# Kernel optimization log

Measured on AMD Instinct MI355X. Metric: run time of the kernel, lower is better.

## Reference

```python
import jax, jax.numpy as jnp
import numpy as np

B, C, H, W = 32, 512, 32, 32
N = H * W            # seq_len = 1024
HEADS = 8
DH = C // HEADS      # 64
K = 256              # linformer low-rank
EPS = 1e-5


def setup_inputs() -> dict:
    key = jax.random.key(0)
    ks = jax.random.split(key, 10)
    s = 0.02
    return {
        "x": jax.random.normal(ks[0], (B, C, H, W), dtype=jnp.float32),
        "pos": jax.random.normal(ks[1], (1, N, C), dtype=jnp.float32),
        "ln_g": jnp.ones((C,), dtype=jnp.float32),
        "ln_b": jnp.zeros((C,), dtype=jnp.float32),
        "Wq": jax.random.normal(ks[2], (C, C), dtype=jnp.float32) * s,
        "Wk": jax.random.normal(ks[3], (C, C), dtype=jnp.float32) * s,
        "Wv": jax.random.normal(ks[4], (C, C), dtype=jnp.float32) * s,
        "proj_k": jax.random.normal(ks[5], (N, K), dtype=jnp.float32) * s,
        "proj_v": jax.random.normal(ks[6], (N, K), dtype=jnp.float32) * s,
        "Wo": jax.random.normal(ks[7], (C, C), dtype=jnp.float32) * s,
        "bo": jnp.zeros((C,), dtype=jnp.float32),
    }


def reference(x, pos, ln_g, ln_b, Wq, Wk, Wv, proj_k, proj_v, Wo, bo):
    b, c, h, w = x.shape
    n = h * w
    # b c h w -> b (h w) c
    xf = x.reshape(b, c, n).transpose(0, 2, 1) + pos
    # LayerNorm (biased variance, eps=1e-5) + ReLU; dropout = identity (eval)
    mu = xf.mean(-1, keepdims=True)
    var = jnp.var(xf, axis=-1, keepdims=True)
    y = (xf - mu) * jax.lax.rsqrt(var + EPS) * ln_g + ln_b
    y = jax.nn.relu(y)
    # Linformer self-attention
    q = y @ Wq                                   # [b,n,c]
    k_ = jnp.einsum('bnd,nk->bkd', y @ Wk, proj_k)  # [b,K,c]
    v_ = jnp.einsum('bnd,nk->bkd', y @ Wv, proj_v)  # [b,K,c]
    q = q.reshape(b, n, HEADS, DH)
    k_ = k_.reshape(b, K, HEADS, DH)
    v_ = v_.reshape(b, K, HEADS, DH)
    dots = jnp.einsum('bnhd,bkhd->bhnk', q, k_) * (DH ** -0.5)
    attn = jax.nn.softmax(dots, axis=-1)
    out = jnp.einsum('bhnk,bkhd->bnhd', attn, v_).reshape(b, n, c)
    out = out @ Wo + bo
    # residual with (x + pos), then back to b c h w
    out = out + xf
    return out.transpose(0, 2, 1).reshape(b, c, h, w)
```

## Files before the change

kernel.cpp:

```cpp
#include <hip/hip_runtime.h>
#include <hip/hip_bf16.h>
#include <cstdint>

#define BB  32
#define CC  512
#define NN  1024
#define HH  8
#define DHH 64
#define KR  256

using f32x4  = __attribute__((ext_vector_type(4))) float;
using f32x16 = __attribute__((ext_vector_type(16))) float;
using bf16x8 = __attribute__((ext_vector_type(8))) __bf16;
using u32x4  = __attribute__((ext_vector_type(4))) unsigned int;

__device__ __forceinline__ unsigned short f2bf(float f) {
  unsigned int u = __float_as_uint(f);
  u += 0x7fffu + ((u >> 16) & 1u);
  return (unsigned short)(u >> 16);
}

__device__ __forceinline__ unsigned int pknat(float a, float b) {
  unsigned short ua = __builtin_bit_cast(unsigned short, (__bf16)a);
  unsigned short ub = __builtin_bit_cast(unsigned short, (__bf16)b);
  return (unsigned int)ua | ((unsigned int)ub << 16);
}

__device__ __forceinline__ void gload16(const void* gsrc, void* ldst) {
  __builtin_amdgcn_global_load_lds(
      (const __attribute__((address_space(1))) unsigned int*)gsrc,
      (__attribute__((address_space(3))) unsigned int*)ldst, 16, 0, 0);
}

__global__ __launch_bounds__(256) void transcvt_all(
    const float* __restrict__ w0, const float* __restrict__ w1,
    const float* __restrict__ w2, const float* __restrict__ w3,
    const float* __restrict__ p0, const float* __restrict__ p1,
    unsigned short* __restrict__ d0, unsigned short* __restrict__ d1,
    unsigned short* __restrict__ d2, unsigned short* __restrict__ d3,
    unsigned short* __restrict__ e0, unsigned short* __restrict__ e1) {
  const int m = blockIdx.y;
  const float* src = m==0?w0:m==1?w1:m==2?w2:m==3?w3:m==4?p0:p1;
  unsigned short* dst = m==0?d0:m==1?d1:m==2?d2:m==3?d3:m==4?e0:e1;
  const int R = (m < 4) ? 512 : 1024;
  const int logC = (m < 4) ? 9 : 8;
  int idx = blockIdx.x * 256 + threadIdx.x;
  int r = idx >> logC, c = idx & ((1 << logC) - 1);
  dst[(size_t)c * R + r] = f2bf(src[idx]);
}

__global__ __launch_bounds__(256) void ln_relu_kernel(
    const float* __restrict__ x, const float* __restrict__ pos,
    const float* __restrict__ g, const float* __restrict__ bta,
    unsigned short* __restrict__ y, unsigned short* __restrict__ yT) {
  __shared__ float tile[16][516];
  __shared__ float smu[16], srs[16];
  const int b = blockIdx.y, n0 = blockIdx.x * 16;
  const int tid = threadIdx.x;
  const float* xb = x + (size_t)b * CC * NN;

  #pragma unroll
  for (int i = 0; i < 32; ++i) {
    int e = i * 256 + tid;
    int c = e >> 4, nl = e & 15;
    tile[nl][c] = xb[(size_t)c * NN + n0 + nl];
  }
  __syncthreads();

  const int r = tid >> 4, l16 = tid & 15;
  float s = 0.f, s2 = 0.f;
  #pragma unroll
  for (int i = 0; i < 32; ++i) {
    int c = l16 + i * 16;
    float v = tile[r][c] + pos[(size_t)(n0 + r) * CC + c];
    s += v; s2 += v * v;
  }
  #pragma unroll
  for (int d = 1; d < 16; d <<= 1) { s += __shfl_xor(s, d); s2 += __shfl_xor(s2, d); }
  if (l16 == 0) {
    float mu = s * (1.f / 512.f);
    float var = s2 * (1.f / 512.f) - mu * mu;
    smu[r] = mu;
    srs[r] = rsqrtf(var + 1e-5f);
  }
  __syncthreads();

  unsigned short* yb = y + ((size_t)b * NN + n0) * CC;
  #pragma unroll
  for (int rr = 0; rr < 16; ++rr) {
    float mu = smu[rr], rs = srs[rr];
    #pragma unroll
    for (int c = tid; c < CC; c += 256) {
      float v = tile[rr][c] + pos[(size_t)(n0 + rr) * CC + c];
      float o = (v - mu) * rs * g[c] + bta[c];
      o = o > 0.f ? o : 0.f;
      yb[(size_t)rr * CC + c] = f2bf(o);
      tile[rr][c] = o;
    }
  }
  __syncthreads();

  unsigned short* ytb = yT + (size_t)b * CC * NN + n0;
  #pragma unroll
  for (int cc = tid; cc < CC; cc += 256) {
    unsigned int pk8[8];
    #pragma unroll
    for (int p = 0; p < 8; ++p)
      pk8[p] = (unsigned int)f2bf(tile[2 * p][cc]) |
               ((unsigned int)f2bf(tile[2 * p + 1][cc]) << 16);
    *reinterpret_cast<uint4*>(&ytb[(size_t)cc * NN])     = *reinterpret_cast<uint4*>(&pk8[0]);
    *reinterpret_cast<uint4*>(&ytb[(size_t)cc * NN + 8]) = *reinterpret_cast<uint4*>(&pk8[4]);
  }
}

template <int MODE>
__global__ __launch_bounds__(256) void gemm_tn(
    const unsigned short* __restrict__ A, int lda, long long strideA,
    const unsigned short* __restrict__ Bt, int ldb, long long strideB,
    unsigned short* __restrict__ Cb, long long strideC,
    int Nn, int Kk, int TB,
    const float* __restrict__ xres, const float* __restrict__ posres,
    const float* __restrict__ bias, float* __restrict__ outF) {
  __shared__ __align__(16) unsigned short aL[2][128 * 64];
  __shared__ __align__(16) unsigned short bL[2][128 * 64];
  const int mb = blockIdx.x * 128, nb = blockIdx.y * 128, zb = blockIdx.z;
  A  += (size_t)strideA * zb;
  Bt += (size_t)strideB * zb;
  if (MODE == 0 || MODE == 1) Cb += (size_t)strideC * zb;
  const int tid  = threadIdx.x;
  const int lane = tid & 63;
  const int wave = tid >> 6;
  const int wm = (wave >> 1) * 64, wn = (wave & 1) * 64;
  const int sr = lane >> 3;
  const int scw = lane & 7;
  f32x4 acc[4][4] = {};

  auto stage = [&](int buf, int k0) {
    #pragma unroll
    for (int i = 0; i < 4; ++i) {
      int row = wave * 32 + i * 8 + sr;
      int ca = scw ^ (row & 7);
      gload16(&A [(size_t)(mb + row) * lda + k0 + ca * 8], &aL[buf][(wave * 32 + i * 8) * 64]);
      gload16(&Bt[(size_t)(nb + row) * ldb + k0 + ca * 8], &bL[buf][(wave * 32 + i * 8) * 64]);
    }
  };

  const int nt = Kk >> 6;
  stage(0, 0);
  __syncthreads();

  for (int t = 0; t < nt; ++t) {
    const int buf = t & 1;
    if (t + 1 < nt) stage(buf ^ 1, (t + 1) << 6);

    bf16x8 af[2][4], bfv[2][4];
    #pragma unroll
    for (int ks = 0; ks < 2; ++ks)
      #pragma unroll
      for (int i = 0; i < 4; ++i) {
        int ra = wm + i * 16 + (lane & 15);
        int rb = wn + i * 16 + (lane & 15);
        int kc = ks * 4 + (lane >> 4);
        af[ks][i]  = *reinterpret_cast<const bf16x8*>(&aL[buf][ra * 64 + (kc ^ (ra & 7)) * 8]);
        bfv[ks][i] = *reinterpret_cast<const bf16x8*>(&bL[buf][rb * 64 + (kc ^ (rb & 7)) * 8]);
      }
    #pragma unroll
    for (int ks = 0; ks < 2; ++ks)
      #pragma unroll
      for (int i = 0; i < 4; ++i)
        #pragma unroll
        for (int j = 0; j < 4; ++j)
          acc[i][j] = __builtin_amdgcn_mfma_f32_16x16x32_bf16(af[ks][i], bfv[ks][j], acc[i][j], 0, 0, 0);
    __syncthreads();
  }

  #pragma unroll
  for (int i = 0; i < 4; ++i) {
    const int r0 = mb + wm + i * 16 + ((lane >> 4) << 2);
    #pragma unroll
    for (int j = 0; j < 4; ++j) {
      const int col = nb + wn + j * 16 + (lane & 15);
      if (MODE == 0) {
        #pragma unroll
        for (int t = 0; t < 4; ++t)
          Cb[(size_t)(r0 + t) * Nn + col] = f2bf(acc[i][j][t]);
      } else if (MODE == 1) {
        unsigned int lo = (unsigned int)f2bf(acc[i][j][0]) | ((unsigned int)f2bf(acc[i][j][1]) << 16);
        unsigned int hi = (unsigned int)f2bf(acc[i][j][2]) | ((unsigned int)f2bf(acc[i][j][3]) << 16);
        size_t addr = (size_t)col * TB + (r0 % TB);
        uint2 u; u.x = lo; u.y = hi;
        *reinterpret_cast<uint2*>(&Cb[addr]) = u;
      } else {
        const int bb = r0 >> 10, t0 = r0 & 1023;
        const size_t base = ((size_t)bb * CC + col) * NN + t0;
        float4 xv = *reinterpret_cast<const float4*>(&xres[base]);
        float bcol = bias[col];
        float4 ov;
        ov.x = acc[i][j][0] + bcol + xv.x + posres[(size_t)(t0 + 0) * CC + col];
        ov.y = acc[i][j][1] + bcol + xv.y + posres[(size_t)(t0 + 1) * CC + col];
        ov.z = acc[i][j][2] + bcol + xv.z + posres[(size_t)(t0 + 2) * CC + col];
        ov.w = acc[i][j][3] + bcol + xv.w + posres[(size_t)(t0 + 3) * CC + col];
        *reinterpret_cast<float4*>(&outF[base]) = ov;
      }
    }
  }
}

__global__ __launch_bounds__(256, 2) void attn_kernel(
    const unsigned short* __restrict__ q,
    const unsigned short* __restrict__ kB,
    const unsigned short* __restrict__ vT,
    unsigned short* __restrict__ O) {
  __shared__ __align__(16) unsigned short smem[32768];
  const int wgid = blockIdx.x;
  const int grp  = wgid & 255;
  const int tg   = wgid >> 8;
  const int h = grp & 7, b = grp >> 3;
  const int wave = threadIdx.x >> 6, lane = threadIdx.x & 63;
  const int t32 = lane & 31, g2 = lane >> 5;
  const int tokb = tg * 128 + wave * 32;

  const unsigned short* qp = q + ((size_t)(b * NN + tokb + t32)) * CC + h * DHH + g2 * 8;
  bf16x8 qf[4];
  #pragma unroll
  for (int st = 0; st < 4; ++st)
    qf[st] = *reinterpret_cast<const bf16x8*>(qp + (size_t)st * 16);

  {
    const unsigned short* kb = kB + ((size_t)b * KR) * CC + h * DHH;
    const int r0w = wave * 64;
    #pragma unroll
    for (int i = 0; i < 8; ++i) {
      int row = r0w + i * 8 + (lane >> 3);
      int sc  = (lane & 7) ^ (row & 7);
      gload16(kb + (size_t)row * CC + sc * 8, &smem[(r0w + i * 8) * 64]);
    }
    const unsigned short* vb = vT + ((size_t)b * CC + h * DHH) * KR;
    const int v0w = wave * 16;
    #pragma unroll
    for (int i = 0; i < 8; ++i) {
      int row = v0w + i * 2 + (lane >> 5);
      int sc  = (lane & 31) ^ (row & 7);
      gload16(vb + (size_t)row * KR + sc * 8, &smem[16384 + (v0w + i * 2) * 256]);
    }
  }
  __syncthreads();

  f32x16 s8[8] = {};
  #pragma unroll
  for (int t8 = 0; t8 < 8; ++t8) {
    const int row = t8 * 32 + t32;
    #pragma unroll
    for (int st = 0; st < 4; ++st) {
      int ch = (2 * st + g2) ^ (row & 7);
      bf16x8 kf = *reinterpret_cast<const bf16x8*>(&smem[row * 64 + ch * 8]);
      s8[t8] = __builtin_amdgcn_mfma_f32_32x32x16_bf16(kf, qf[st], s8[t8], 0, 0, 0);
    }
  }

  float m = -1e30f;
  #pragma unroll
  for (int t8 = 0; t8 < 8; ++t8)
    #pragma unroll
    for (int r = 0; r < 16; ++r) m = fmaxf(m, s8[t8][r]);
  m = fmaxf(m, __shfl_xor(m, 32));
  const float cexp = 0.125f * 1.44269504088896f;
  float ls = 0.f;
  #pragma unroll
  for (int t8 = 0; t8 < 8; ++t8)
    #pragma unroll
    for (int r = 0; r < 16; ++r) {
      float p = __builtin_amdgcn_exp2f((s8[t8][r] - m) * cexp);
      s8[t8][r] = p;
      ls += p;
    }
  ls += __shfl_xor(ls, 32);
  float rinv = __builtin_amdgcn_rcpf(ls);

  f32x16 o0 = {}, o1 = {};
  #pragma unroll
  for (int t8 = 0; t8 < 8; ++t8) {
    unsigned int pkd[8];
    #pragma unroll
    for (int qq = 0; qq < 4; ++qq) {
      pkd[qq * 2 + 0] = pknat(s8[t8][4 * qq + 0], s8[t8][4 * qq + 1]);
      pkd[qq * 2 + 1] = pknat(s8[t8][4 * qq + 2], s8[t8][4 * qq + 3]);
    }
    #pragma unroll
    for (int a = 0; a < 2; ++a) {
      const int ks = t8 * 2 + a;
      unsigned int xe0 = pkd[4 * a + 0], xe1 = pkd[4 * a + 1];
      unsigned int xo0 = pkd[4 * a + 2], xo1 = pkd[4 * a + 3];
      unsigned int d0 = g2 ? __shfl_xor(xo0, 32) : xe0;
      unsigned int d1 = g2 ? __shfl_xor(xo1, 32) : xe1;
      unsigned int d2 = g2 ? xo0 : __shfl_xor(xe0, 32);
      unsigned int d3 = g2 ? xo1 : __shfl_xor(xe1, 32);
      u32x4 pv_ = {d0, d1, d2, d3};
      bf16x8 pa = __builtin_bit_cast(bf16x8, pv_);
      #pragma unroll
      for (int dt = 0; dt < 2; ++dt) {
        int row = dt * 32 + t32;
        int ch = (2 * ks + g2) ^ (row & 7);
        bf16x8 bv = *reinterpret_cast<const bf16x8*>(&smem[16384 + row * 256 + ch * 8]);
        if (dt == 0) o0 = __builtin_amdgcn_mfma_f32_32x32x16_bf16(pa, bv, o0, 0, 0, 0);
        else         o1 = __builtin_amdgcn_mfma_f32_32x32x16_bf16(pa, bv, o1, 0, 0, 0);
      }
    }
  }

  unsigned short* Ob = O + ((size_t)(b * NN + tokb)) * CC + h * DHH;
  #pragma unroll
  for (int r = 0; r < 16; ++r) {
    int tl = (r & 3) + 8 * (r >> 2) + 4 * g2;
    float rs = __shfl(rinv, tl);
    Ob[(size_t)tl * CC + t32]      = f2bf(o0[r] * rs);
    Ob[(size_t)tl * CC + 32 + t32] = f2bf(o1[r] * rs);
  }
}

extern "C" void kernel_launch(void* const* d_in, const int* in_sizes, int n_in,
                              void* d_out, int out_size, void* d_ws, size_t ws_size,
                              hipStream_t stream) {
  const float* x    = (const float*)d_in[0];
  const float* pos  = (const float*)d_in[1];
  const float* ln_g = (const float*)d_in[2];
  const float* ln_b = (const float*)d_in[3];
  const float* Wq   = (const float*)d_in[4];
  const float* Wk   = (const float*)d_in[5];
  const float* Wv   = (const float*)d_in[6];
  const float* pk   = (const float*)d_in[7];
  const float* pv   = (const float*)d_in[8];
  const float* Wo   = (const float*)d_in[9];
  const float* bo   = (const float*)d_in[10];
  float* out = (float*)d_out;

  unsigned short* ws = (unsigned short*)d_ws;
  size_t off = 0;
  auto alloc = [&](size_t elems) { unsigned short* p = ws + off; off += elems; return p; };
  unsigned short* WqT     = alloc(512 * 512);
  unsigned short* WkT     = alloc(512 * 512);
  unsigned short* WvT     = alloc(512 * 512);
  unsigned short* WoT     = alloc(512 * 512);
  unsigned short* projcat = alloc((size_t)512 * 1024);
  unsigned short* yB      = alloc((size_t)32768 * 512);
  unsigned short* yT      = alloc((size_t)32 * 512 * 1024);
  unsigned short* qB      = alloc((size_t)32768 * 512);
  unsigned short* zB      = alloc((size_t)32 * 512 * 512);
  unsigned short* kBuf    = alloc((size_t)32 * 256 * 512);
  unsigned short* vTB     = alloc((size_t)32 * 512 * 256);
  unsigned short* OB      = alloc((size_t)32768 * 512);

  transcvt_all<<<dim3(1024, 6), 256, 0, stream>>>(
      Wq, Wk, Wv, Wo, pk, pv,
      WqT, WkT, WvT, WoT, projcat, projcat + (size_t)256 * 1024);

  ln_relu_kernel<<<dim3(64, 32), 256, 0, stream>>>(x, pos, ln_g, ln_b, yB, yT);

  gemm_tn<0><<<dim3(256, 4), 256, 0, stream>>>(
      yB, 512, 0, WqT, 512, 0, qB, 0, 512, 512, 0, nullptr, nullptr, nullptr, nullptr);

  gemm_tn<0><<<dim3(4, 4, 32), 256, 0, stream>>>(
      projcat, 1024, 0, yT, 1024, (long long)512 * 1024, zB, (long long)512 * 512,
      512, 1024, 0, nullptr, nullptr, nullptr, nullptr);

  gemm_tn<0><<<dim3(2, 4, 32), 256, 0, stream>>>(
      zB, 512, (long long)512 * 512, WkT, 512, 0, kBuf, (long long)256 * 512,
      512, 512, 0, nullptr, nullptr, nullptr, nullptr);

  gemm_tn<1><<<dim3(2, 4, 32), 256, 0, stream>>>(
      zB + (size_t)256 * 512, 512, (long long)512 * 512, WvT, 512, 0,
      vTB, (long long)512 * 256, 512, 512, 256, nullptr, nullptr, nullptr, nullptr);

  attn_kernel<<<dim3(2048, 1, 1), 256, 0, stream>>>(qB, kBuf, vTB, OB);

  gemm_tn<2><<<dim3(256, 4), 256, 0, stream>>>(
      OB, 512, 0, WoT, 512, 0, nullptr, 0, 512, 512, 0, x, pos, bo, out);
}
```

Measured before the change: 228.6 us.

## Shrink GEMM K-tile, stage epilogues through LDS, transpose output GEMM for coalescing

The GEMM K-step drops from 64 to 32 with a new 4-way swizzle, which cuts LDS use and may allow more resident blocks. MODE 0 and MODE 1 epilogues now stage the bf16 tile in shared memory and write 16-byte coalesced rows instead of scattered 2-byte or 8-byte stores. The output projection swaps its operands so that consecutive lanes map to consecutive tokens, and reads a pre-transposed fp32 pos copy made by a new kernel, so the NCHW residual stores become coalesced. LayerNorm now adds pos into the tile once instead of reading it twice. Grid dimensions are swapped to match the new block-index mapping, and the changes add an extra kernel launch and more loop iterations per GEMM.

```diff
diff --git a/kernel.cpp b/kernel.cpp
--- a/kernel.cpp
+++ b/kernel.cpp
@@ -49,6 +49,13 @@
   dst[(size_t)c * R + r] = f2bf(src[idx]);
 }
 
+__global__ __launch_bounds__(256) void posT_kernel(
+    const float* __restrict__ pos, float* __restrict__ posT) {
+  int idx = blockIdx.x * 256 + threadIdx.x;
+  int c = idx >> 10, n = idx & 1023;
+  posT[idx] = pos[(size_t)n * CC + c];
+}
+
 __global__ __launch_bounds__(256) void ln_relu_kernel(
     const float* __restrict__ x, const float* __restrict__ pos,
     const float* __restrict__ g, const float* __restrict__ bta,
@@ -66,13 +73,18 @@
     tile[nl][c] = xb[(size_t)c * NN + n0 + nl];
   }
   __syncthreads();
+  #pragma unroll
+  for (int i = 0; i < 32; ++i) {
+    int nl = i >> 1, c = (i & 1) * 256 + tid;
+    tile[nl][c] += pos[(size_t)(n0 + nl) * CC + c];
+  }
+  __syncthreads();
 
   const int r = tid >> 4, l16 = tid & 15;
   float s = 0.f, s2 = 0.f;
   #pragma unroll
   for (int i = 0; i < 32; ++i) {
-    int c = l16 + i * 16;
-    float v = tile[r][c] + pos[(size_t)(n0 + r) * CC + c];
+    float v = tile[r][l16 + i * 16];
     s += v; s2 += v * v;
   }
   #pragma unroll
@@ -91,7 +103,7 @@
     float mu = smu[rr], rs = srs[rr];
     #pragma unroll
     for (int c = tid; c < CC; c += 256) {
-      float v = tile[rr][c] + pos[(size_t)(n0 + rr) * CC + c];
+      float v = tile[rr][c];
       float o = (v - mu) * rs * g[c] + bta[c];
       o = o > 0.f ? o : 0.f;
       yb[(size_t)rr * CC + c] = f2bf(o);
@@ -119,11 +131,12 @@
     const unsigned short* __restrict__ Bt, int ldb, long long strideB,
     unsigned short* __restrict__ Cb, long long strideC,
     int Nn, int Kk, int TB,
-    const float* __restrict__ xres, const float* __restrict__ posres,
+    const float* __restrict__ xres, const float* __restrict__ posT,
     const float* __restrict__ bias, float* __restrict__ outF) {
-  __shared__ __align__(16) unsigned short aL[2][128 * 64];
-  __shared__ __align__(16) unsigned short bL[2][128 * 64];
-  const int mb = blockIdx.x * 128, nb = blockIdx.y * 128, zb = blockIdx.z;
+  __shared__ __align__(16) unsigned short sh[17408];
+  unsigned short* aL = sh;
+  unsigned short* bL = sh + 8192;
+  const int nb = blockIdx.x * 128, mb = blockIdx.y * 128, zb = blockIdx.z;
   A  += (size_t)strideA * zb;
   Bt += (size_t)strideB * zb;
   if (MODE == 0 || MODE == 1) Cb += (size_t)strideC * zb;
@@ -131,77 +144,87 @@
   const int lane = tid & 63;
   const int wave = tid >> 6;
   const int wm = (wave >> 1) * 64, wn = (wave & 1) * 64;
-  const int sr = lane >> 3;
-  const int scw = lane & 7;
+  const int sr  = lane >> 2;
+  const int scw = lane & 3;
   f32x4 acc[4][4] = {};
 
   auto stage = [&](int buf, int k0) {
     #pragma unroll
-    for (int i = 0; i < 4; ++i) {
-      int row = wave * 32 + i * 8 + sr;
-      int ca = scw ^ (row & 7);
-      gload16(&A [(size_t)(mb + row) * lda + k0 + ca * 8], &aL[buf][(wave * 32 + i * 8) * 64]);
-      gload16(&Bt[(size_t)(nb + row) * ldb + k0 + ca * 8], &bL[buf][(wave * 32 + i * 8) * 64]);
+    for (int i = 0; i < 2; ++i) {
+      int rbase = wave * 32 + i * 16;
+      int row = rbase + sr;
+      int ca = scw ^ ((row ^ (row >> 2)) & 3);
+      gload16(&A [(size_t)(mb + row) * lda + k0 + ca * 8], &aL[buf * 4096 + rbase * 32]);
+      gload16(&Bt[(size_t)(nb + row) * ldb + k0 + ca * 8], &bL[buf * 4096 + rbase * 32]);
     }
   };
 
-  const int nt = Kk >> 6;
+  const int nt = Kk >> 5;
   stage(0, 0);
   __syncthreads();
 
   for (int t = 0; t < nt; ++t) {
     const int buf = t & 1;
-    if (t + 1 < nt) stage(buf ^ 1, (t + 1) << 6);
-
-    bf16x8 af[2][4], bfv[2][4];
-    #pragma unroll
-    for (int ks = 0; ks < 2; ++ks)
+    if (t + 1 < nt) stage(buf ^ 1, (t + 1) << 5);
+
+    bf16x8 af[4], bfv[4];
+    const int kc = lane >> 4;
+    #pragma unroll
+    for (int i = 0; i < 4; ++i) {
+      int ra = wm + i * 16 + (lane & 15);
+      int rb = wn + i * 16 + (lane & 15);
+      af[i]  = *reinterpret_cast<const bf16x8*>(&aL[buf * 4096 + ra * 32 + (kc ^ ((ra ^ (ra >> 2)) & 3)) * 8]);
+      bfv[i] = *reinterpret_cast<const bf16x8*>(&bL[buf * 4096 + rb * 32 + (kc ^ ((rb ^ (rb >> 2)) & 3)) * 8]);
+    }
+    #pragma unroll
+    for (int i = 0; i < 4; ++i)
       #pragma unroll
-      for (int i = 0; i < 4; ++i) {
-        int ra = wm + i * 16 + (lane & 15);
-        int rb = wn + i * 16 + (lane & 15);
-        int kc = ks * 4 + (lane >> 4);
-        af[ks][i]  = *reinterpret_cast<const bf16x8*>(&aL[buf][ra * 64 + (kc ^ (ra & 7)) * 8]);
-        bfv[ks][i] = *reinterpret_cast<const bf16x8*>(&bL[buf][rb * 64 + (kc ^ (rb & 7)) * 8]);
+      for (int j = 0; j < 4; ++j)
+        acc[i][j] = __builtin_amdgcn_mfma_f32_16x16x32_bf16(af[i], bfv[j], acc[i][j], 0, 0, 0);
+    __syncthreads();
+  }
+
+  if (MODE == 2) {
+    #pragma unroll
+    for (int i = 0; i < 4; ++i) {
+      const int c0 = mb + wm + i * 16 + ((lane >> 4) << 2);
+      #pragma unroll
+      for (int j = 0; j < 4; ++j) {
+        const int col = nb + wn + j * 16 + (lane & 15);
+        const int bcell = col >> 10, t0 = col & 1023;
+        #pragma unroll
+        for (int t = 0; t < 4; ++t) {
+          const int c = c0 + t;
+          const size_t base = ((size_t)bcell * CC + c) * NN + t0;
+          outF[base] = acc[i][j][t] + bias[c] + xres[base] + posT[(size_t)c * NN + t0];
+        }
       }
-    #pragma unroll
-    for (int ks = 0; ks < 2; ++ks)
+    }
+  } else {
+    auto Ct = (unsigned short (*)[136])sh;
+    #pragma unroll
+    for (int i = 0; i < 4; ++i) {
+      const int r0 = wm + i * 16 + ((lane >> 4) << 2);
       #pragma unroll
-      for (int i = 0; i < 4; ++i)
+      for (int j = 0; j < 4; ++j) {
+        const int cl = wn + j * 16 + (lane & 15);
         #pragma unroll
-        for (int j = 0; j < 4; ++j)
-          acc[i][j] = __builtin_amdgcn_mfma_f32_16x16x32_bf16(af[ks][i], bfv[ks][j], acc[i][j], 0, 0, 0);
+        for (int t = 0; t < 4; ++t) {
+          if (MODE == 0) Ct[r0 + t][cl] = f2bf(acc[i][j][t]);
+          else           Ct[cl][r0 + t] = f2bf(acc[i][j][t]);
+        }
+      }
+    }
     __syncthreads();
-  }
-
-  #pragma unroll
-  for (int i = 0; i < 4; ++i) {
-    const int r0 = mb + wm + i * 16 + ((lane >> 4) << 2);
-    #pragma unroll
-    for (int j = 0; j < 4; ++j) {
-      const int col = nb + wn + j * 16 + (lane & 15);
-      if (MODE == 0) {
-        #pragma unroll
-        for (int t = 0; t < 4; ++t)
-          Cb[(size_t)(r0 + t) * Nn + col] = f2bf(acc[i][j][t]);
-      } else if (MODE == 1) {
-        unsigned int lo = (unsigned int)f2bf(acc[i][j][0]) | ((unsigned int)f2bf(acc[i][j][1]) << 16);
-        unsigned int hi = (unsigned int)f2bf(acc[i][j][2]) | ((unsigned int)f2bf(acc[i][j][3]) << 16);
-        size_t addr = (size_t)col * TB + (r0 % TB);
-        uint2 u; u.x = lo; u.y = hi;
-        *reinterpret_cast<uint2*>(&Cb[addr]) = u;
-      } else {
-        const int bb = r0 >> 10, t0 = r0 & 1023;
-        const size_t base = ((size_t)bb * CC + col) * NN + t0;
-        float4 xv = *reinterpret_cast<const float4*>(&xres[base]);
-        float bcol = bias[col];
-        float4 ov;
-        ov.x = acc[i][j][0] + bcol + xv.x + posres[(size_t)(t0 + 0) * CC + col];
-        ov.y = acc[i][j][1] + bcol + xv.y + posres[(size_t)(t0 + 1) * CC + col];
-        ov.z = acc[i][j][2] + bcol + xv.z + posres[(size_t)(t0 + 2) * CC + col];
-        ov.w = acc[i][j][3] + bcol + xv.w + posres[(size_t)(t0 + 3) * CC + col];
-        *reinterpret_cast<float4*>(&outF[base]) = ov;
-      }
+    const int rr = tid >> 4, ch = tid & 15;
+    #pragma unroll
+    for (int it = 0; it < 8; ++it) {
+      const int r = it * 16 + rr;
+      uint4 v = *reinterpret_cast<const uint4*>(&Ct[r][ch * 8]);
+      if (MODE == 0)
+        *reinterpret_cast<uint4*>(&Cb[(size_t)(mb + r) * Nn + nb + ch * 8]) = v;
+      else
+        *reinterpret_cast<uint4*>(&Cb[(size_t)(nb + r) * TB + mb + ch * 8]) = v;
     }
   }
 }
@@ -342,6 +365,7 @@
   unsigned short* WvT     = alloc(512 * 512);
   unsigned short* WoT     = alloc(512 * 512);
   unsigned short* projcat = alloc((size_t)512 * 1024);
+  float*          posTb   = (float*)alloc((size_t)512 * 1024 * 2);
   unsigned short* yB      = alloc((size_t)32768 * 512);
   unsigned short* yT      = alloc((size_t)32 * 512 * 1024);
   unsigned short* qB      = alloc((size_t)32768 * 512);
@@ -353,26 +377,27 @@
   transcvt_all<<<dim3(1024, 6), 256, 0, stream>>>(
       Wq, Wk, Wv, Wo, pk, pv,
       WqT, WkT, WvT, WoT, projcat, projcat + (size_t)256 * 1024);
+  posT_kernel<<<2048, 256, 0, stream>>>(pos, posTb);
 
   ln_relu_kernel<<<dim3(64, 32), 256, 0, stream>>>(x, pos, ln_g, ln_b, yB, yT);
 
-  gemm_tn<0><<<dim3(256, 4), 256, 0, stream>>>(
+  gemm_tn<0><<<dim3(4, 256), 256, 0, stream>>>(
       yB, 512, 0, WqT, 512, 0, qB, 0, 512, 512, 0, nullptr, nullptr, nullptr, nullptr);
 
   gemm_tn<0><<<dim3(4, 4, 32), 256, 0, stream>>>(
       projcat, 1024, 0, yT, 1024, (long long)512 * 1024, zB, (long long)512 * 512,
       512, 1024, 0, nullptr, nullptr, nullptr, nullptr);
 
-  gemm_tn<0><<<dim3(2, 4, 32), 256, 0, stream>>>(
+  gemm_tn<0><<<dim3(4, 2, 32), 256, 0, stream>>>(
       zB, 512, (long long)512 * 512, WkT, 512, 0, kBuf, (long long)256 * 512,
       512, 512, 0, nullptr, nullptr, nullptr, nullptr);
 
-  gemm_tn<1><<<dim3(2, 4, 32), 256, 0, stream>>>(
+  gemm_tn<1><<<dim3(4, 2, 32), 256, 0, stream>>>(
       zB + (size_t)256 * 512, 512, (long long)512 * 512, WvT, 512, 0,
       vTB, (long long)512 * 256, 512, 512, 256, nullptr, nullptr, nullptr, nullptr);
 
   attn_kernel<<<dim3(2048, 1, 1), 256, 0, stream>>>(qB, kBuf, vTB, OB);
 
   gemm_tn<2><<<dim3(256, 4), 256, 0, stream>>>(
-      OB, 512, 0, WoT, 512, 0, nullptr, 0, 512, 512, 0, x, pos, bo, out);
-}
+      WoT, 512, 0, OB, 512, 0, nullptr, 0, 32768, 512, 0, x, posTb, bo, out);
+}
```

Result: no change. 229.2 us (+0.3%).
